# Kernel optimization log

Measured on AMD Instinct MI355X. Metric: run time of the kernel, lower is better.

Reference implementation:

```python
import jax, jax.numpy as jnp
import numpy as np

N = 30000      # input points
M = 7500       # sampled queries = floor(N * ratio), ratio=0.25
K = 16         # neighbors per query
D_X = 64       # input feature dim
D_REL = 64     # point_pos_nn output dim
D_F = D_X + D_REL  # fij_hat dim = 128


def setup_inputs() -> dict:
    key = jax.random.key(0)
    ks = jax.random.split(key, 6)
    x = jax.random.normal(ks[0], (N, D_X), jnp.float32)
    pos = jax.random.normal(ks[1], (N, 3), jnp.float32)
    idx = jax.random.randint(ks[2], (M,), 0, N)
    W_pos = jax.random.normal(ks[3], (10, D_REL), jnp.float32) / jnp.sqrt(10.0)
    b_pos = jnp.zeros((D_REL,), jnp.float32)
    W_att = jax.random.normal(ks[4], (D_F, D_F), jnp.float32) / jnp.sqrt(float(D_F))
    b_att = jnp.zeros((D_F,), jnp.float32)
    W_glob = jax.random.normal(ks[5], (D_F, D_F), jnp.float32) / jnp.sqrt(float(D_F))
    b_glob = jnp.zeros((D_F,), jnp.float32)
    return {"x": x, "pos": pos, "idx": idx, "W_pos": W_pos, "b_pos": b_pos,
            "W_att": W_att, "b_att": b_att, "W_glob": W_glob, "b_glob": b_glob}


def reference(x, pos, idx, W_pos, b_pos, W_att, b_att, W_glob, b_glob):
    # --- KNN: brute-force squared distances from sampled queries to all points ---
    pos_q = pos[idx]                                         # [M, 3]
    d2 = ((pos_q * pos_q).sum(-1)[:, None]
          + (pos * pos).sum(-1)[None, :]
          - 2.0 * pos_q @ pos.T)                             # [M, N]
    _, nbr = jax.lax.top_k(-d2, K)                           # [M, K] neighbor indices

    # --- Local Spatial Encoding (message) ---
    pos_j = pos[nbr]                                         # [M, K, 3]
    pos_i = jnp.broadcast_to(pos_q[:, None, :], pos_j.shape) # [M, K, 3]
    vij = pos_i - pos_j                                      # [M, K, 3]
    dij = jnp.linalg.norm(vij, axis=-1, keepdims=True)       # [M, K, 1]
    rel = jnp.concatenate([pos_i, pos_j, vij, dij], axis=-1) # [M, K, 10]
    rij = jax.nn.relu(rel @ W_pos + b_pos)                   # [M, K, D_REL]

    # --- Attentive pooling ---
    fij = jnp.concatenate([x[nbr], rij], axis=-1)            # [M, K, D_F]
    g = fij @ W_att + b_att                                  # [M, K, D_F]
    s = jax.nn.softmax(g, axis=-1)                           # softmax over feature dim
    aggr = jnp.mean(s * fij, axis=1)                         # mean over K neighbors -> [M, D_F]

    # --- global_nn (update) ---
    return jax.nn.relu(aggr @ W_glob + b_glob)               # [M, D_F]
```

## Files before the change

### kernel.cpp

```cpp
#include <hip/hip_runtime.h>
#include <stdint.h>

#define KQ    8
#define CAP   512
#define KNN_T 256
#define KNB   16

typedef short short8 __attribute__((ext_vector_type(8)));
typedef float floatx4 __attribute__((ext_vector_type(4)));
typedef float floatx2 __attribute__((ext_vector_type(2)));

__device__ __forceinline__ unsigned short f2bf(float x) {
  union { float f; uint32_t u; } v; v.f = x;
  uint32_t u = v.u + 0x7FFFu + ((v.u >> 16) & 1u);
  return (unsigned short)(u >> 16);
}
__device__ __forceinline__ float bf2f(unsigned short b) {
  return __uint_as_float(((uint32_t)b) << 16);
}

static __device__ __forceinline__ floatx2 fma2(floatx2 a, floatx2 b, floatx2 c) {
#if __has_builtin(__builtin_elementwise_fma)
  return __builtin_elementwise_fma(a, b, c);
#else
  floatx2 r; r[0] = fmaf(a[0], b[0], c[0]); r[1] = fmaf(a[1], b[1], c[1]);
  return r;
#endif
}
static __device__ __forceinline__ floatx2 min2(floatx2 a, floatx2 b) {
#if __has_builtin(__builtin_elementwise_min)
  return __builtin_elementwise_min(a, b);
#else
  floatx2 r; r[0] = fminf(a[0], b[0]); r[1] = fminf(a[1], b[1]);
  return r;
#endif
}
static __device__ __forceinline__ floatx2 sp2(float v) {
  floatx2 r; r[0] = v; r[1] = v; return r;
}

__global__ void prep_kernel(const float* __restrict__ x,
                            const float* __restrict__ pos,
                            const float* __restrict__ W_att,
                            unsigned short* __restrict__ xb,
                            float4* __restrict__ pos4,
                            float* __restrict__ pospk,
                            unsigned short* __restrict__ Wt, int N, int Npad2) {
  int id = blockIdx.x * 256 + threadIdx.x;
  int nx8 = N * 8;
  if (id < nx8) {
    const float4* src = (const float4*)x + (size_t)id * 2;
    float4 a = src[0], b = src[1];
    short8 v;
    v[0] = (short)f2bf(a.x); v[1] = (short)f2bf(a.y);
    v[2] = (short)f2bf(a.z); v[3] = (short)f2bf(a.w);
    v[4] = (short)f2bf(b.x); v[5] = (short)f2bf(b.y);
    v[6] = (short)f2bf(b.z); v[7] = (short)f2bf(b.w);
    *(short8*)(xb + (size_t)id * 8) = v;
  } else if (id < nx8 + Npad2) {
    int j = id - nx8;
    float px = 0.f, py = 0.f, pz = 0.f, pp = 3.0e38f;
    if (j < N) {
      px = pos[3 * j]; py = pos[3 * j + 1]; pz = pos[3 * j + 2];
      pp = fmaf(px, px, fmaf(py, py, pz * pz));
      pos4[j] = make_float4(px, py, pz, pp);
    }
    int pair = j >> 1, h = j & 1;
    float* dst = pospk + (size_t)pair * 8;
    dst[0 + h] = px; dst[2 + h] = py; dst[4 + h] = pz; dst[6 + h] = pp;
  } else if (id < nx8 + Npad2 + 128 * 128) {
    int t = id - nx8 - Npad2;
    int c = t >> 7, f = t & 127;
    Wt[f * 128 + c] = f2bf(W_att[t]);
  }
}

__global__ __launch_bounds__(KNN_T) void knn_kernel(
    const float4* __restrict__ pos4, const float4* __restrict__ pospk4,
    const int* __restrict__ idx, int* __restrict__ nbr, int Npad2, int M) {
  __shared__ uint32_t cand[KQ][CAP];
  __shared__ int cnt[KQ];
  __shared__ float gmin[KQ][16];
  __shared__ float tau_s[KQ];
  __shared__ float4 qpos_s[KQ];

  const int tid = threadIdx.x;
  const int q0  = blockIdx.x * KQ;
  const int iters = Npad2 >> 9;

  float sx[KQ], sy[KQ], sz[KQ];
#pragma unroll
  for (int qi = 0; qi < KQ; ++qi) {
    int m = q0 + qi; if (m >= M) m = M - 1;
    float4 qp = pos4[idx[m]];
    sx[qi] = -2.f * qp.x; sy[qi] = -2.f * qp.y; sz[qi] = -2.f * qp.z;
    if (tid == qi) qpos_s[qi] = qp;
  }
  if (tid < KQ) cnt[tid] = 0;

  floatx2 tmn[KQ];
#pragma unroll
  for (int qi = 0; qi < KQ; ++qi) tmn[qi] = sp2(3.4e38f);
  {
    float4 a = pospk4[tid * 2], b = pospk4[tid * 2 + 1];
    for (int it = 0; it < iters; ++it) {
      float4 an = a, bn = b;
      if (it + 1 < iters) {
        int nb = (it + 1) * 512 + tid * 2;
        an = pospk4[nb]; bn = pospk4[nb + 1];
      }
      floatx2 X, Y, Z, W;
      X[0] = a.x; X[1] = a.y; Y[0] = a.z; Y[1] = a.w;
      Z[0] = b.x; Z[1] = b.y; W[0] = b.z; W[1] = b.w;
#pragma unroll
      for (int qi = 0; qi < KQ; ++qi) {
        floatx2 t = fma2(sp2(sx[qi]), X,
                         fma2(sp2(sy[qi]), Y, fma2(sp2(sz[qi]), Z, W)));
        tmn[qi] = min2(tmn[qi], t);
      }
      a = an; b = bn;
    }
  }
#pragma unroll
  for (int qi = 0; qi < KQ; ++qi) {
    float v = fminf(tmn[qi][0], tmn[qi][1]);
    v = fminf(v, __shfl_xor(v, 1));
    v = fminf(v, __shfl_xor(v, 2));
    v = fminf(v, __shfl_xor(v, 4));
    v = fminf(v, __shfl_xor(v, 8));
    if ((tid & 15) == 0) gmin[qi][tid >> 4] = v;
  }
  __syncthreads();
  if (tid < KQ) {
    float t = gmin[tid][0];
#pragma unroll
    for (int g = 1; g < 16; ++g) t = fmaxf(t, gmin[tid][g]);
    tau_s[tid] = t + fabsf(t) * 1e-6f + 1e-7f;
  }
  __syncthreads();
  float tau[KQ];
#pragma unroll
  for (int qi = 0; qi < KQ; ++qi) tau[qi] = tau_s[qi];

  {
    float4 a = pospk4[tid * 2], b = pospk4[tid * 2 + 1];
    for (int it = 0; it < iters; ++it) {
      float4 an = a, bn = b;
      if (it + 1 < iters) {
        int nb = (it + 1) * 512 + tid * 2;
        an = pospk4[nb]; bn = pospk4[nb + 1];
      }
      floatx2 X, Y, Z, W;
      X[0] = a.x; X[1] = a.y; Y[0] = a.z; Y[1] = a.w;
      Z[0] = b.x; Z[1] = b.y; W[0] = b.z; W[1] = b.w;
      const int j0 = (it * 256 + tid) * 2;
#pragma unroll
      for (int qi = 0; qi < KQ; ++qi) {
        floatx2 t = fma2(sp2(sx[qi]), X,
                         fma2(sp2(sy[qi]), Y, fma2(sp2(sz[qi]), Z, W)));
        if (fminf(t[0], t[1]) <= tau[qi]) {
          if (t[0] <= tau[qi]) {
            int sl = atomicAdd(&cnt[qi], 1);
            if (sl < CAP) cand[qi][sl] = (uint32_t)j0;
          }
          if (t[1] <= tau[qi]) {
            int sl = atomicAdd(&cnt[qi], 1);
            if (sl < CAP) cand[qi][sl] = (uint32_t)(j0 + 1);
          }
        }
      }
      a = an; b = bn;
    }
  }
  __syncthreads();

  const int wv = tid >> 6, ln = tid & 63;
#pragma unroll
  for (int i = 0; i < 2; ++i) {
    int ql = wv * 2 + i;
    int mq = q0 + ql;
    int nc = cnt[ql]; if (nc > CAP) nc = CAP;
    float4 qp = qpos_s[ql];
    unsigned long long c[CAP / 64];
#pragma unroll
    for (int ch = 0; ch < CAP / 64; ++ch) c[ch] = ~0ull;
#pragma unroll
    for (int ch = 0; ch < CAP / 64; ++ch) {
      int s = ch * 64 + ln;
      if (s < nc) {
        uint32_t j = cand[ql][s];
        float4 pj = pos4[j];
        float dot = fmaf(qp.x, pj.x, fmaf(qp.y, pj.y, qp.z * pj.z));
        float tt  = fmaf(-2.f, dot, pj.w);
        float d2  = fmaxf(qp.w + tt, 0.f);
        c[ch] = ((unsigned long long)__float_as_uint(d2) << 32) | j;
      }
    }
#pragma unroll
    for (int r = 0; r < KNB; ++r) {
      unsigned long long mn = c[0];
#pragma unroll
      for (int ch = 1; ch < CAP / 64; ++ch) mn = (c[ch] < mn) ? c[ch] : mn;
#pragma unroll
      for (int off = 1; off < 64; off <<= 1) {
        unsigned long long o = __shfl_xor(mn, off);
        mn = (o < mn) ? o : mn;
      }
      if (mq < M && ln == 0) nbr[mq * KNB + r] = (int)(uint32_t)mn;
#pragma unroll
      for (int ch = 0; ch < CAP / 64; ++ch)
        if (c[ch] == mn) c[ch] = ~0ull;
    }
  }
}

__global__ __launch_bounds__(256) void mid_kernel(
    const unsigned short* __restrict__ xb, const float4* __restrict__ pos4,
    const int* __restrict__ idx, const float* __restrict__ W_pos,
    const float* __restrict__ b_pos, const unsigned short* __restrict__ Wt,
    const float* __restrict__ b_att, const int* __restrict__ nbr,
    float* __restrict__ aggr, int M) {
  __shared__ __align__(16) unsigned short fijb[8][16][136];
  __shared__ int nbr_s[128];
  __shared__ float4 qpos_s[8];

  const int tid = threadIdx.x;
  const int wid = tid >> 6, lane = tid & 63;
  const int col = lane & 15, quad = lane >> 4;
  const int b = blockIdx.x;

  if (tid < 128) {
    int mq = b * 8 + (tid >> 4); if (mq >= M) mq = M - 1;
    nbr_s[tid] = nbr[mq * 16 + (tid & 15)];
  }
  if (tid < 8) {
    int mq = b * 8 + tid; if (mq >= M) mq = M - 1;
    qpos_s[tid] = pos4[idx[mq]];
  }
  float wp[10];
#pragma unroll
  for (int t = 0; t < 10; ++t) wp[t] = W_pos[t * 64 + lane];
  float bp = b_pos[lane];
  __syncthreads();

  {
    int rr = tid >> 1, h = tid & 1;
    int jn = nbr_s[rr];
    const short8* src = (const short8*)(xb + ((size_t)jn << 6) + (h << 5));
    short8 v0 = src[0], v1 = src[1], v2 = src[2], v3 = src[3];
    short8* dst = (short8*)&fijb[rr >> 4][rr & 15][h * 32];
    dst[0] = v0; dst[1] = v1; dst[2] = v2; dst[3] = v3;
  }
#pragma unroll
  for (int qi = 0; qi < 2; ++qi) {
    int q = wid * 2 + qi;
    float4 qp = qpos_s[q];
#pragma unroll 4
    for (int k = 0; k < 16; ++k) {
      int jn = nbr_s[q * 16 + k];
      float4 pj = pos4[jn];
      float vx = qp.x - pj.x, vy = qp.y - pj.y, vz = qp.z - pj.z;
      float dd = sqrtf(fmaf(vx, vx, fmaf(vy, vy, vz * vz)));
      float r = bp;
      r = fmaf(qp.x, wp[0], r); r = fmaf(qp.y, wp[1], r); r = fmaf(qp.z, wp[2], r);
      r = fmaf(pj.x, wp[3], r); r = fmaf(pj.y, wp[4], r); r = fmaf(pj.z, wp[5], r);
      r = fmaf(vx, wp[6], r);  r = fmaf(vy, wp[7], r);  r = fmaf(vz, wp[8], r);
      r = fmaf(dd, wp[9], r);
      r = fmaxf(r, 0.f);
      fijb[q][k][64 + lane] = f2bf(r);
    }
  }
  __syncthreads();

#pragma unroll 1
  for (int qi = 0; qi < 2; ++qi) {
    int q = wid * 2 + qi;
    int mq = b * 8 + q;

    short8 af[4];
#pragma unroll
    for (int cs = 0; cs < 4; ++cs)
      af[cs] = *(const short8*)&fijb[q][col][cs * 32 + quad * 8];

    floatx4 acc[8];
#pragma unroll
    for (int ft = 0; ft < 8; ++ft) {
      float bav = b_att[ft * 16 + col];
      floatx4 a = {bav, bav, bav, bav};
#pragma unroll
      for (int cs = 0; cs < 4; ++cs) {
        short8 bfrag =
            *(const short8*)&Wt[(ft * 16 + col) * 128 + cs * 32 + quad * 8];
        a = __builtin_amdgcn_mfma_f32_16x16x32_bf16(af[cs], bfrag, a, 0, 0, 0);
      }
      acc[ft] = a;
    }

    float rowmax[4], rowinv[4];
#pragma unroll
    for (int r = 0; r < 4; ++r) {
      float mx = acc[0][r];
#pragma unroll
      for (int ft = 1; ft < 8; ++ft) mx = fmaxf(mx, acc[ft][r]);
      mx = fmaxf(mx, __shfl_xor(mx, 1));
      mx = fmaxf(mx, __shfl_xor(mx, 2));
      mx = fmaxf(mx, __shfl_xor(mx, 4));
      mx = fmaxf(mx, __shfl_xor(mx, 8));
      float sm = 0.f;
#pragma unroll
      for (int ft = 0; ft < 8; ++ft) sm += __expf(acc[ft][r] - mx);
      sm += __shfl_xor(sm, 1);
      sm += __shfl_xor(sm, 2);
      sm += __shfl_xor(sm, 4);
      sm += __shfl_xor(sm, 8);
      rowmax[r] = mx;
      rowinv[r] = 1.0f / sm;
    }

#pragma unroll
    for (int ft = 0; ft < 8; ++ft) {
      float ap = 0.f;
#pragma unroll
      for (int r = 0; r < 4; ++r) {
        float s = __expf(acc[ft][r] - rowmax[r]) * rowinv[r];
        float fv = bf2f(fijb[q][quad * 4 + r][ft * 16 + col]);
        ap = fmaf(s, fv, ap);
      }
      ap += __shfl_xor(ap, 16);
      ap += __shfl_xor(ap, 32);
      if (quad == 0 && mq < M)
        aggr[mq * 128 + ft * 16 + col] = ap * (1.0f / 16.0f);
    }
  }
}

__global__ __launch_bounds__(256) void out_kernel(
    const float* __restrict__ aggr, const float* __restrict__ W_glob,
    const float* __restrict__ b_glob, float* __restrict__ out, int M) {
  __shared__ float ag[16][128];
  const int tid = threadIdx.x;
  const int mbase = blockIdx.x * 16;
  for (int s = tid; s < 16 * 128; s += 256) {
    int r = s >> 7, cc = s & 127;
    int m = mbase + r;
    ((float*)ag)[s] = (m < M) ? aggr[m * 128 + cc] : 0.0f;
  }
  __syncthreads();
  const int f = tid & 127, h = tid >> 7;
  float acc[8];
  float bg = b_glob[f];
#pragma unroll
  for (int i = 0; i < 8; ++i) acc[i] = bg;
  for (int c = 0; c < 128; c += 4) {
    float w0 = W_glob[(c + 0) * 128 + f];
    float w1 = W_glob[(c + 1) * 128 + f];
    float w2 = W_glob[(c + 2) * 128 + f];
    float w3 = W_glob[(c + 3) * 128 + f];
#pragma unroll
    for (int i = 0; i < 8; ++i) {
      const floatx4 a4 = *(const floatx4*)&ag[h * 8 + i][c];
      acc[i] += a4[0] * w0 + a4[1] * w1 + a4[2] * w2 + a4[3] * w3;
    }
  }
#pragma unroll
  for (int i = 0; i < 8; ++i) {
    int m = mbase + h * 8 + i;
    if (m < M) out[m * 128 + f] = fmaxf(acc[i], 0.0f);
  }
}

extern "C" void kernel_launch(void* const* d_in, const int* in_sizes, int n_in,
                              void* d_out, int out_size, void* d_ws,
                              size_t ws_size, hipStream_t stream) {
  const float* x      = (const float*)d_in[0];
  const float* pos    = (const float*)d_in[1];
  const int*   idx    = (const int*)d_in[2];
  const float* W_pos  = (const float*)d_in[3];
  const float* b_pos  = (const float*)d_in[4];
  const float* W_att  = (const float*)d_in[5];
  const float* b_att  = (const float*)d_in[6];
  const float* W_glob = (const float*)d_in[7];
  const float* b_glob = (const float*)d_in[8];
  float* out = (float*)d_out;

  const int N = in_sizes[1] / 3;
  const int M = in_sizes[2];
  const int Npad2 = (N + 511) & ~511;

  char* ws = (char*)d_ws;
  size_t o = 0;
  float4* pos4 = (float4*)(ws + o);               o += ((size_t)N * 16 + 255) & ~(size_t)255;
  unsigned short* xb = (unsigned short*)(ws + o); o += ((size_t)N * 128 + 255) & ~(size_t)255;
  float* pospk = (float*)(ws + o);                o += ((size_t)Npad2 * 16 + 255) & ~(size_t)255;
  unsigned short* Wt = (unsigned short*)(ws + o); o += (128 * 128 * 2 + 255) & ~(size_t)255;
  int* nbr = (int*)(ws + o);                      o += (((size_t)M * KNB * 4) + 255) & ~(size_t)255;
  float* aggr = (float*)(ws + o);

  int prep_ids = N * 8 + Npad2 + 128 * 128;
  prep_kernel<<<(prep_ids + 255) / 256, 256, 0, stream>>>(
      x, pos, W_att, xb, pos4, pospk, Wt, N, Npad2);
  knn_kernel<<<(M + KQ - 1) / KQ, KNN_T, 0, stream>>>(
      pos4, (const float4*)pospk, idx, nbr, Npad2, M);
  mid_kernel<<<(M + 7) / 8, 256, 0, stream>>>(xb, pos4, idx, W_pos, b_pos, Wt,
                                              b_att, nbr, aggr, M);
  out_kernel<<<(M + 15) / 16, 256, 0, stream>>>(aggr, W_glob, b_glob, out, M);
}
```

Before: 229.4 us.

## Split KNN search across point chunks with a separate top-k merge kernel

The KNN kernel now adds a second grid dimension, so each block scans only one quarter of the points for its 8 queries. Each chunk-block writes its own top-16 candidates as packed (distance, index) keys into a partial buffer. A new merge kernel then picks the final 16 neighbours per query from the 64 partial candidates with a wave-level min reduction. The aim is more blocks and a shorter serial scan per block, so the GPU is better filled. The cost is repeated per-block threshold and selection work, an extra launch, and extra workspace traffic.

```diff
diff --git a/kernel.cpp b/kernel.cpp
--- a/kernel.cpp
+++ b/kernel.cpp
@@ -5,6 +5,7 @@
 #define CAP   512
 #define KNN_T 256
 #define KNB   16
+#define NCH   4
 
 typedef short short8 __attribute__((ext_vector_type(8)));
 typedef float floatx4 __attribute__((ext_vector_type(4)));
@@ -77,7 +78,8 @@
 
 __global__ __launch_bounds__(KNN_T) void knn_kernel(
     const float4* __restrict__ pos4, const float4* __restrict__ pospk4,
-    const int* __restrict__ idx, int* __restrict__ nbr, int Npad2, int M) {
+    const int* __restrict__ idx, unsigned long long* __restrict__ part,
+    int Npad2, int M) {
   __shared__ uint32_t cand[KQ][CAP];
   __shared__ int cnt[KQ];
   __shared__ float gmin[KQ][16];
@@ -86,7 +88,8 @@
 
   const int tid = threadIdx.x;
   const int q0  = blockIdx.x * KQ;
-  const int iters = Npad2 >> 9;
+  const int c0  = blockIdx.y * (Npad2 >> 2);
+  const int iters = Npad2 >> 11;
 
   float sx[KQ], sy[KQ], sz[KQ];
 #pragma unroll
@@ -102,11 +105,11 @@
 #pragma unroll
   for (int qi = 0; qi < KQ; ++qi) tmn[qi] = sp2(3.4e38f);
   {
-    float4 a = pospk4[tid * 2], b = pospk4[tid * 2 + 1];
+    float4 a = pospk4[c0 + tid * 2], b = pospk4[c0 + tid * 2 + 1];
     for (int it = 0; it < iters; ++it) {
       float4 an = a, bn = b;
       if (it + 1 < iters) {
-        int nb = (it + 1) * 512 + tid * 2;
+        int nb = c0 + (it + 1) * 512 + tid * 2;
         an = pospk4[nb]; bn = pospk4[nb + 1];
       }
       floatx2 X, Y, Z, W;
@@ -143,17 +146,17 @@
   for (int qi = 0; qi < KQ; ++qi) tau[qi] = tau_s[qi];
 
   {
-    float4 a = pospk4[tid * 2], b = pospk4[tid * 2 + 1];
+    float4 a = pospk4[c0 + tid * 2], b = pospk4[c0 + tid * 2 + 1];
     for (int it = 0; it < iters; ++it) {
       float4 an = a, bn = b;
       if (it + 1 < iters) {
-        int nb = (it + 1) * 512 + tid * 2;
+        int nb = c0 + (it + 1) * 512 + tid * 2;
         an = pospk4[nb]; bn = pospk4[nb + 1];
       }
       floatx2 X, Y, Z, W;
       X[0] = a.x; X[1] = a.y; Y[0] = a.z; Y[1] = a.w;
       Z[0] = b.x; Z[1] = b.y; W[0] = b.z; W[1] = b.w;
-      const int j0 = (it * 256 + tid) * 2;
+      const int j0 = c0 + (it * 256 + tid) * 2;
 #pragma unroll
       for (int qi = 0; qi < KQ; ++qi) {
         floatx2 t = fma2(sp2(sx[qi]), X,
@@ -206,11 +209,33 @@
         unsigned long long o = __shfl_xor(mn, off);
         mn = (o < mn) ? o : mn;
       }
-      if (mq < M && ln == 0) nbr[mq * KNB + r] = (int)(uint32_t)mn;
+      if (mq < M && ln == 0)
+        part[((size_t)mq << 6) + (blockIdx.y << 4) + r] = mn;
 #pragma unroll
       for (int ch = 0; ch < CAP / 64; ++ch)
         if (c[ch] == mn) c[ch] = ~0ull;
     }
+  }
+}
+
+__global__ __launch_bounds__(256) void merge_kernel(
+    const unsigned long long* __restrict__ part, int* __restrict__ nbr,
+    int M) {
+  const int tid = threadIdx.x;
+  const int wv = tid >> 6, ln = tid & 63;
+  const int m = blockIdx.x * 4 + wv;
+  if (m >= M) return;
+  unsigned long long c = part[((size_t)m << 6) + ln];
+#pragma unroll
+  for (int r = 0; r < KNB; ++r) {
+    unsigned long long mn = c;
+#pragma unroll
+    for (int off = 1; off < 64; off <<= 1) {
+      unsigned long long o = __shfl_xor(mn, off);
+      mn = (o < mn) ? o : mn;
+    }
+    if (ln == 0) nbr[m * KNB + r] = (int)(uint32_t)mn;
+    if (c == mn) c = ~0ull;
   }
 }
 
@@ -385,7 +410,7 @@
 
   const int N = in_sizes[1] / 3;
   const int M = in_sizes[2];
-  const int Npad2 = (N + 511) & ~511;
+  const int Npad2 = (N + (NCH * 512 - 1)) & ~(NCH * 512 - 1);
 
   char* ws = (char*)d_ws;
   size_t o = 0;
@@ -394,13 +419,17 @@
   float* pospk = (float*)(ws + o);                o += ((size_t)Npad2 * 16 + 255) & ~(size_t)255;
   unsigned short* Wt = (unsigned short*)(ws + o); o += (128 * 128 * 2 + 255) & ~(size_t)255;
   int* nbr = (int*)(ws + o);                      o += (((size_t)M * KNB * 4) + 255) & ~(size_t)255;
+  unsigned long long* part = (unsigned long long*)(ws + o);
+  o += (((size_t)M * NCH * KNB * 8) + 255) & ~(size_t)255;
   float* aggr = (float*)(ws + o);
 
   int prep_ids = N * 8 + Npad2 + 128 * 128;
   prep_kernel<<<(prep_ids + 255) / 256, 256, 0, stream>>>(
       x, pos, W_att, xb, pos4, pospk, Wt, N, Npad2);
-  knn_kernel<<<(M + KQ - 1) / KQ, KNN_T, 0, stream>>>(
-      pos4, (const float4*)pospk, idx, nbr, Npad2, M);
+  dim3 knn_grid((M + KQ - 1) / KQ, NCH);
+  knn_kernel<<<knn_grid, KNN_T, 0, stream>>>(
+      pos4, (const float4*)pospk, idx, part, Npad2, M);
+  merge_kernel<<<(M + 3) / 4, 256, 0, stream>>>(part, nbr, M);
   mid_kernel<<<(M + 7) / 8, 256, 0, stream>>>(xb, pos4, idx, W_pos, b_pos, Wt,
                                               b_att, nbr, aggr, M);
   out_kernel<<<(M + 15) / 16, 256, 0, stream>>>(aggr, W_glob, b_glob, out, M);
```

New measurement: 299.5 us. +30.6%, slower.

## Halve queries per KNN block and process four points per thread per iteration

Applied to the files above, without the earlier changes.

The KNN block now handles 4 queries instead of 8, so the grid doubles and each wave handles one query in the selection phase. Each thread now loads four packed pairs per iteration, covering 1024 points, which halves the iteration count and doubles ILP per loop. Padding changes to a multiple of 1024 and candidate capacity drops to 256. Points are re-streamed twice as often across blocks, and the smaller candidate buffer raises the risk of overflow.

```diff
diff --git a/kernel.cpp b/kernel.cpp
--- a/kernel.cpp
+++ b/kernel.cpp
@@ -1,8 +1,8 @@
 #include <hip/hip_runtime.h>
 #include <stdint.h>
 
-#define KQ    8
-#define CAP   512
+#define KQ    4
+#define CAP   256
 #define KNN_T 256
 #define KNB   16
 
@@ -86,7 +86,7 @@
 
   const int tid = threadIdx.x;
   const int q0  = blockIdx.x * KQ;
-  const int iters = Npad2 >> 9;
+  const int iters = Npad2 >> 10;
 
   float sx[KQ], sy[KQ], sz[KQ];
 #pragma unroll
@@ -102,23 +102,30 @@
 #pragma unroll
   for (int qi = 0; qi < KQ; ++qi) tmn[qi] = sp2(3.4e38f);
   {
-    float4 a = pospk4[tid * 2], b = pospk4[tid * 2 + 1];
+    int base = tid * 4;
+    float4 a = pospk4[base], b = pospk4[base + 1];
+    float4 c4 = pospk4[base + 2], d4 = pospk4[base + 3];
     for (int it = 0; it < iters; ++it) {
-      float4 an = a, bn = b;
+      float4 an = a, bn = b, cn = c4, dn = d4;
       if (it + 1 < iters) {
-        int nb = (it + 1) * 512 + tid * 2;
-        an = pospk4[nb]; bn = pospk4[nb + 1];
-      }
-      floatx2 X, Y, Z, W;
-      X[0] = a.x; X[1] = a.y; Y[0] = a.z; Y[1] = a.w;
-      Z[0] = b.x; Z[1] = b.y; W[0] = b.z; W[1] = b.w;
+        int nb = (it + 1) * 1024 + tid * 4;
+        an = pospk4[nb];     bn = pospk4[nb + 1];
+        cn = pospk4[nb + 2]; dn = pospk4[nb + 3];
+      }
+      floatx2 X0, Y0, Z0, W0, X1, Y1, Z1, W1;
+      X0[0] = a.x;  X0[1] = a.y;  Y0[0] = a.z;  Y0[1] = a.w;
+      Z0[0] = b.x;  Z0[1] = b.y;  W0[0] = b.z;  W0[1] = b.w;
+      X1[0] = c4.x; X1[1] = c4.y; Y1[0] = c4.z; Y1[1] = c4.w;
+      Z1[0] = d4.x; Z1[1] = d4.y; W1[0] = d4.z; W1[1] = d4.w;
 #pragma unroll
       for (int qi = 0; qi < KQ; ++qi) {
-        floatx2 t = fma2(sp2(sx[qi]), X,
-                         fma2(sp2(sy[qi]), Y, fma2(sp2(sz[qi]), Z, W)));
-        tmn[qi] = min2(tmn[qi], t);
-      }
-      a = an; b = bn;
+        floatx2 t0 = fma2(sp2(sx[qi]), X0,
+                          fma2(sp2(sy[qi]), Y0, fma2(sp2(sz[qi]), Z0, W0)));
+        floatx2 t1 = fma2(sp2(sx[qi]), X1,
+                          fma2(sp2(sy[qi]), Y1, fma2(sp2(sz[qi]), Z1, W1)));
+        tmn[qi] = min2(tmn[qi], min2(t0, t1));
+      }
+      a = an; b = bn; c4 = cn; d4 = dn;
     }
   }
 #pragma unroll
@@ -143,41 +150,56 @@
   for (int qi = 0; qi < KQ; ++qi) tau[qi] = tau_s[qi];
 
   {
-    float4 a = pospk4[tid * 2], b = pospk4[tid * 2 + 1];
+    int base = tid * 4;
+    float4 a = pospk4[base], b = pospk4[base + 1];
+    float4 c4 = pospk4[base + 2], d4 = pospk4[base + 3];
     for (int it = 0; it < iters; ++it) {
-      float4 an = a, bn = b;
+      float4 an = a, bn = b, cn = c4, dn = d4;
       if (it + 1 < iters) {
-        int nb = (it + 1) * 512 + tid * 2;
-        an = pospk4[nb]; bn = pospk4[nb + 1];
-      }
-      floatx2 X, Y, Z, W;
-      X[0] = a.x; X[1] = a.y; Y[0] = a.z; Y[1] = a.w;
-      Z[0] = b.x; Z[1] = b.y; W[0] = b.z; W[1] = b.w;
-      const int j0 = (it * 256 + tid) * 2;
+        int nb = (it + 1) * 1024 + tid * 4;
+        an = pospk4[nb];     bn = pospk4[nb + 1];
+        cn = pospk4[nb + 2]; dn = pospk4[nb + 3];
+      }
+      floatx2 X0, Y0, Z0, W0, X1, Y1, Z1, W1;
+      X0[0] = a.x;  X0[1] = a.y;  Y0[0] = a.z;  Y0[1] = a.w;
+      Z0[0] = b.x;  Z0[1] = b.y;  W0[0] = b.z;  W0[1] = b.w;
+      X1[0] = c4.x; X1[1] = c4.y; Y1[0] = c4.z; Y1[1] = c4.w;
+      Z1[0] = d4.x; Z1[1] = d4.y; W1[0] = d4.z; W1[1] = d4.w;
+      const int j0 = it * 1024 + tid * 4;
 #pragma unroll
       for (int qi = 0; qi < KQ; ++qi) {
-        floatx2 t = fma2(sp2(sx[qi]), X,
-                         fma2(sp2(sy[qi]), Y, fma2(sp2(sz[qi]), Z, W)));
-        if (fminf(t[0], t[1]) <= tau[qi]) {
-          if (t[0] <= tau[qi]) {
+        floatx2 t0 = fma2(sp2(sx[qi]), X0,
+                          fma2(sp2(sy[qi]), Y0, fma2(sp2(sz[qi]), Z0, W0)));
+        floatx2 t1 = fma2(sp2(sx[qi]), X1,
+                          fma2(sp2(sy[qi]), Y1, fma2(sp2(sz[qi]), Z1, W1)));
+        float m01 = fminf(fminf(t0[0], t0[1]), fminf(t1[0], t1[1]));
+        if (m01 <= tau[qi]) {
+          if (t0[0] <= tau[qi]) {
             int sl = atomicAdd(&cnt[qi], 1);
             if (sl < CAP) cand[qi][sl] = (uint32_t)j0;
           }
-          if (t[1] <= tau[qi]) {
+          if (t0[1] <= tau[qi]) {
             int sl = atomicAdd(&cnt[qi], 1);
             if (sl < CAP) cand[qi][sl] = (uint32_t)(j0 + 1);
           }
+          if (t1[0] <= tau[qi]) {
+            int sl = atomicAdd(&cnt[qi], 1);
+            if (sl < CAP) cand[qi][sl] = (uint32_t)(j0 + 2);
+          }
+          if (t1[1] <= tau[qi]) {
+            int sl = atomicAdd(&cnt[qi], 1);
+            if (sl < CAP) cand[qi][sl] = (uint32_t)(j0 + 3);
+          }
         }
       }
-      a = an; b = bn;
+      a = an; b = bn; c4 = cn; d4 = dn;
     }
   }
   __syncthreads();
 
   const int wv = tid >> 6, ln = tid & 63;
-#pragma unroll
-  for (int i = 0; i < 2; ++i) {
-    int ql = wv * 2 + i;
+  {
+    int ql = wv;
     int mq = q0 + ql;
     int nc = cnt[ql]; if (nc > CAP) nc = CAP;
     float4 qp = qpos_s[ql];
@@ -385,7 +407,7 @@
 
   const int N = in_sizes[1] / 3;
   const int M = in_sizes[2];
-  const int Npad2 = (N + 511) & ~511;
+  const int Npad2 = (N + 1023) & ~1023;
 
   char* ws = (char*)d_ws;
   size_t o = 0;
```

Result: slower. 255.9 us (+11.6%).

## Double KNN block size to 512 threads with two-deep prefetch, one query per wave

Applied to the files above, without the earlier changes.

Raises the KNN block from 256 to 512 threads, so each of 8 waves owns one query in the selection phase instead of two. The point scan now strides 1024 points per iteration, and the padding is raised to a multiple of 1024 to match. The one-step register prefetch becomes two-deep to hide more global-load latency. The group minimum now reduces over 32 lanes, giving 16 groups, so tau is still an upper bound covering at least 16 candidates. The cost is higher per-block register and occupancy pressure and a little more padded work.

```diff
diff --git a/kernel.cpp b/kernel.cpp
--- a/kernel.cpp
+++ b/kernel.cpp
@@ -3,7 +3,7 @@
 
 #define KQ    8
 #define CAP   512
-#define KNN_T 256
+#define KNN_T 512
 #define KNB   16
 
 typedef short short8 __attribute__((ext_vector_type(8)));
@@ -86,7 +86,7 @@
 
   const int tid = threadIdx.x;
   const int q0  = blockIdx.x * KQ;
-  const int iters = Npad2 >> 9;
+  const int iters = Npad2 >> 10;
 
   float sx[KQ], sy[KQ], sz[KQ];
 #pragma unroll
@@ -98,27 +98,29 @@
   }
   if (tid < KQ) cnt[tid] = 0;
 
+  const int f0 = tid * 2;
+
   floatx2 tmn[KQ];
 #pragma unroll
   for (int qi = 0; qi < KQ; ++qi) tmn[qi] = sp2(3.4e38f);
   {
-    float4 a = pospk4[tid * 2], b = pospk4[tid * 2 + 1];
+    float4 a0 = pospk4[f0], b0 = pospk4[f0 + 1];
+    int i1 = (1 < iters) ? 1 : 0;
+    float4 a1 = pospk4[i1 * 1024 + f0], b1 = pospk4[i1 * 1024 + f0 + 1];
     for (int it = 0; it < iters; ++it) {
-      float4 an = a, bn = b;
-      if (it + 1 < iters) {
-        int nb = (it + 1) * 512 + tid * 2;
-        an = pospk4[nb]; bn = pospk4[nb + 1];
-      }
+      int itn = (it + 2 < iters) ? (it + 2) : it;
+      int fn = itn * 1024 + f0;
+      float4 a2 = pospk4[fn], b2 = pospk4[fn + 1];
       floatx2 X, Y, Z, W;
-      X[0] = a.x; X[1] = a.y; Y[0] = a.z; Y[1] = a.w;
-      Z[0] = b.x; Z[1] = b.y; W[0] = b.z; W[1] = b.w;
+      X[0] = a0.x; X[1] = a0.y; Y[0] = a0.z; Y[1] = a0.w;
+      Z[0] = b0.x; Z[1] = b0.y; W[0] = b0.z; W[1] = b0.w;
 #pragma unroll
       for (int qi = 0; qi < KQ; ++qi) {
         floatx2 t = fma2(sp2(sx[qi]), X,
                          fma2(sp2(sy[qi]), Y, fma2(sp2(sz[qi]), Z, W)));
         tmn[qi] = min2(tmn[qi], t);
       }
-      a = an; b = bn;
+      a0 = a1; b0 = b1; a1 = a2; b1 = b2;
     }
   }
 #pragma unroll
@@ -128,7 +130,8 @@
     v = fminf(v, __shfl_xor(v, 2));
     v = fminf(v, __shfl_xor(v, 4));
     v = fminf(v, __shfl_xor(v, 8));
-    if ((tid & 15) == 0) gmin[qi][tid >> 4] = v;
+    v = fminf(v, __shfl_xor(v, 16));
+    if ((tid & 31) == 0) gmin[qi][tid >> 5] = v;
   }
   __syncthreads();
   if (tid < KQ) {
@@ -143,17 +146,17 @@
   for (int qi = 0; qi < KQ; ++qi) tau[qi] = tau_s[qi];
 
   {
-    float4 a = pospk4[tid * 2], b = pospk4[tid * 2 + 1];
+    float4 a0 = pospk4[f0], b0 = pospk4[f0 + 1];
+    int i1 = (1 < iters) ? 1 : 0;
+    float4 a1 = pospk4[i1 * 1024 + f0], b1 = pospk4[i1 * 1024 + f0 + 1];
     for (int it = 0; it < iters; ++it) {
-      float4 an = a, bn = b;
-      if (it + 1 < iters) {
-        int nb = (it + 1) * 512 + tid * 2;
-        an = pospk4[nb]; bn = pospk4[nb + 1];
-      }
+      int itn = (it + 2 < iters) ? (it + 2) : it;
+      int fn = itn * 1024 + f0;
+      float4 a2 = pospk4[fn], b2 = pospk4[fn + 1];
       floatx2 X, Y, Z, W;
-      X[0] = a.x; X[1] = a.y; Y[0] = a.z; Y[1] = a.w;
-      Z[0] = b.x; Z[1] = b.y; W[0] = b.z; W[1] = b.w;
-      const int j0 = (it * 256 + tid) * 2;
+      X[0] = a0.x; X[1] = a0.y; Y[0] = a0.z; Y[1] = a0.w;
+      Z[0] = b0.x; Z[1] = b0.y; W[0] = b0.z; W[1] = b0.w;
+      const int j0 = (it * 512 + tid) * 2;
 #pragma unroll
       for (int qi = 0; qi < KQ; ++qi) {
         floatx2 t = fma2(sp2(sx[qi]), X,
@@ -169,15 +172,14 @@
           }
         }
       }
-      a = an; b = bn;
+      a0 = a1; b0 = b1; a1 = a2; b1 = b2;
     }
   }
   __syncthreads();
 
   const int wv = tid >> 6, ln = tid & 63;
-#pragma unroll
-  for (int i = 0; i < 2; ++i) {
-    int ql = wv * 2 + i;
+  {
+    int ql = wv;
     int mq = q0 + ql;
     int nc = cnt[ql]; if (nc > CAP) nc = CAP;
     float4 qp = qpos_s[ql];
@@ -385,7 +387,7 @@
 
   const int N = in_sizes[1] / 3;
   const int M = in_sizes[2];
-  const int Npad2 = (N + 511) & ~511;
+  const int Npad2 = (N + 1023) & ~1023;
 
   char* ws = (char*)d_ws;
   size_t o = 0;
```

Measured after the change: 229.2 us. Within noise of the previous version (-0.1%).
